# Performance work log

Measured on AMD Instinct MI355X. Metric: run time of the kernel, lower is better.

The kernel has to match this reference:

```python
import jax, jax.numpy as jnp
import numpy as np

NK, TH, SHARP, IMW, IMH = 9, 80.0, 2.0, 640.0, 480.0
NOOBJ, OBJ, COORD, CLS_SCALE, SIL = 1.0, 5.0, 1.0, 1.0, 0.6
NA, NC = 1, 13

def corner_conf(pr, gt):
    # pr, gt: [..., 9, 2] normalized corner coords
    scale = jnp.array([IMW, IMH], dtype=pr.dtype)
    d = (gt - pr) * scale
    dist = jnp.sqrt(jnp.sum(d * d, axis=-1))
    c = (jnp.exp(SHARP * (1.0 - dist / TH)) - 1.0) / (np.exp(SHARP) - 1.0)
    return jnp.where(dist < TH, c, 0.0).mean(axis=-1)

def build_targets(pc, target, nH, nW):
    # pc: [nB, nA*nH*nW, 9, 2] detached predicted corners (layout anchor-major, matching torch flatten)
    nB = target.shape[0]
    nL = 2 * NK + 3
    tgt = target.reshape(nB, 50, nL)
    # break on first slot with coord==0 -> valid prefix
    valid = jnp.cumprod((tgt[:, :, 1] != 0).astype(jnp.int32), axis=1).astype(bool)
    gt_c = tgt[:, :, 1:1 + 2 * NK].reshape(nB, 50, NK, 2)
    confs = corner_conf(pc[:, None], gt_c[:, :, None])  # [nB, 50, nAnch]
    cur = jnp.max(jnp.where(valid[:, :, None], confs, 0.0), axis=1)  # running max over targets
    conf_mask = jnp.where(cur > SIL, 0.0, NOOBJ).reshape(nB, NA, nH, nW)
    gi = (tgt[:, :, 1] * nW).astype(jnp.int32)  # int() truncation, coords in (0,1)
    gj = (tgt[:, :, 2] * nH).astype(jnp.int32)
    coord_mask = jnp.zeros((nB, NA, nH, nW), target.dtype)
    cls_mask = jnp.zeros((nB, NA, nH, nW), target.dtype)
    tcls = jnp.zeros((nB, NA, nH, nW), target.dtype)
    b = jnp.arange(nB)
    for t in range(50):  # fixed 50-slot buffer; sequential overwrite preserved
        git = jnp.where(valid[:, t], gi[:, t], nW)  # invalid -> OOB index, dropped
        gjt = gj[:, t]
        coord_mask = coord_mask.at[b, 0, gjt, git].set(1.0, mode='drop')
        conf_mask = conf_mask.at[b, 0, gjt, git].set(OBJ, mode='drop')
        cls_mask = cls_mask.at[b, 0, gjt, git].set(1.0, mode='drop')
        tcls = tcls.at[b, 0, gjt, git].set(tgt[:, t, 0], mode='drop')
    return coord_mask, conf_mask, cls_mask, tcls

def forward(output, distiled_target, target):
    nB, _, nH, nW = output.shape
    out = output.reshape(nB, NA, 19 + NC, nH, nW)
    coords = jnp.concatenate([jax.nn.sigmoid(out[:, :, :2]), out[:, :, 2:18]], axis=2)
    conf = jax.nn.sigmoid(out[:, :, 18])
    cls_logits = out[:, :, 19:]  # [nB, nA, nC, nH, nW]
    gx = jnp.arange(nW, dtype=output.dtype)
    gy = jnp.arange(nH, dtype=output.dtype)
    px = (coords[:, :, 0::2] + gx[None, None, None, None, :]) / nW  # [nB,NA,9,nH,nW]
    py = (coords[:, :, 1::2] + gy[None, None, None, :, None]) / nH
    pc = jnp.stack([px, py], axis=-1)  # [nB,NA,9,nH,nW,2]
    pc = jnp.transpose(pc, (0, 1, 3, 4, 2, 5)).reshape(nB, NA * nH * nW, NK, 2)
    pc = jax.lax.stop_gradient(pc)  # torch uses .data (detached) for build_targets
    coord_mask, conf_mask, cls_mask, tcls = build_targets(pc, target, nH, nW)
    # distilled (teacher) targets replace build_targets' tx*/ty*/tconf
    dt = distiled_target.reshape(nB, NA, 19 + NC, nH, nW)
    tcoords = jnp.concatenate([jax.nn.sigmoid(dt[:, :, :2]), dt[:, :, 2:18]], axis=2)
    tconf = jax.nn.sigmoid(dt[:, :, 18])
    cm = coord_mask[:, :, None]  # broadcast over 18 coord channels
    loss_coord = COORD * 0.5 * jnp.sum(((coords - tcoords) * cm) ** 2)
    loss_conf = 0.5 * jnp.sum(((conf - tconf) * jnp.sqrt(conf_mask)) ** 2)
    logp = jax.nn.log_softmax(cls_logits, axis=2)
    ce = -jnp.take_along_axis(logp, tcls.astype(jnp.int32)[:, :, None], axis=2)[:, :, 0]
    loss_cls = CLS_SCALE * jnp.sum(cls_mask * ce)  # CrossEntropyLoss(size_average=False) on masked cells
    return loss_coord + loss_conf + loss_cls

def setup_inputs():
    key = jax.random.key(0)
    k1, k2, k3, k4 = jax.random.split(key, 4)
    nB, nH, nW = 16, 76, 76
    output = jax.random.normal(k1, (nB, NA * (19 + NC), nH, nW), dtype=jnp.float32)
    distiled_target = jax.random.normal(k2, (nB, NA * (19 + NC), nH, nW), dtype=jnp.float32)
    nL = 2 * NK + 3
    target = jax.random.uniform(k3, (nB, 50 * nL), dtype=jnp.float32, minval=0.02, maxval=0.98)
    cls_col = jax.random.randint(k4, (nB, 50), 0, NC).astype(jnp.float32)
    target = target.at[:, 0::nL].set(cls_col)
    target = target.at[:, 20 * nL:].set(0.0)  # 20 valid objects per image
    return {"output": output, "distiled_target": distiled_target, "target": target}

def reference(output, distiled_target, target):
    return forward(output, distiled_target, target)
```

## Files before the change

kernel.cpp:

```cpp
#include <hip/hip_runtime.h>
#include <math.h>

#define NB    16
#define NH    76
#define NW    76
#define NCELL (NH * NW)
#define NCH   32
#define NKP   9
#define NCLS  13
#define NT    50
#define NLROW 21
#define BLOCK 256
#define CPB   ((NCELL + BLOCK - 1) / BLOCK)

#define INV_EM1 0.15651764274966565f

__device__ __forceinline__ float sigmoidf_(float x) {
    return 1.0f / (1.0f + __expf(-x));
}

__global__ __launch_bounds__(BLOCK) void loss_main(
    const float* __restrict__ out,
    const float* __restrict__ dt,
    const float* __restrict__ tgt,
    float* __restrict__ partial)
{
    __shared__ float sraw[NT * NLROW];
    __shared__ float sgtx[NT * NKP];
    __shared__ float sgty[NT * NKP];
    __shared__ int   sgi[NT], sgj[NT], scls[NT];
    __shared__ int   snv;
    __shared__ float swsum[BLOCK / 64];

    const int b   = blockIdx.y;
    const int tid = threadIdx.x;

    for (int i = tid; i < NT * NLROW; i += BLOCK)
        sraw[i] = tgt[b * NT * NLROW + i];
    __syncthreads();

    if (tid < NT) {
        sgi[tid] = (int)(sraw[tid * NLROW + 1] * (float)NW);
        sgj[tid] = (int)(sraw[tid * NLROW + 2] * (float)NH);
        int c = (int)sraw[tid * NLROW + 0];
        scls[tid] = min(max(c, 0), NCLS - 1);
    }
    if (tid < NT * NKP) {
        int t = tid / NKP, k = tid - t * NKP;
        sgtx[tid] = sraw[t * NLROW + 1 + 2 * k] * 640.0f;
        sgty[tid] = sraw[t * NLROW + 2 + 2 * k] * 480.0f;
    }
    if (tid == 0) {
        int nv = 0;
        while (nv < NT && sraw[nv * NLROW + 1] != 0.0f) nv++;
        snv = nv;
    }
    __syncthreads();

    const int cell = blockIdx.x * BLOCK + tid;
    float total = 0.0f;

    if (cell < NCELL) {
        const int j = cell / NW;
        const int i = cell - j * NW;
        const float fi = (float)i, fj = (float)j;

        const float* ob = out + (size_t)b * NCH * NCELL + cell;
        const float* db = dt  + (size_t)b * NCH * NCELL + cell;

        float px[NKP], py[NKP];
        #pragma unroll
        for (int k = 0; k < NKP; k++) {
            float cx = ob[(2 * k)     * NCELL];
            float cy = ob[(2 * k + 1) * NCELL];
            if (k == 0) { cx = sigmoidf_(cx); cy = sigmoidf_(cy); }
            px[k] = (cx + fi) * (640.0f / 76.0f);
            py[k] = (cy + fj) * (480.0f / 76.0f);
        }
        const float conf  = sigmoidf_(ob[18 * NCELL]);
        const float tconf = sigmoidf_(db[18 * NCELL]);

        const int nv = snv;
        float cur = 0.0f;
        int flag = 0, tcls = 0;
        for (int t = 0; t < nv; t++) {
            if (sgi[t] == i && sgj[t] == j) { flag = 1; tcls = scls[t]; }
            float s = 0.0f;
            #pragma unroll
            for (int k = 0; k < NKP; k++) {
                float dx = sgtx[t * NKP + k] - px[k];
                float dy = sgty[t * NKP + k] - py[k];
                float dist = sqrtf(dx * dx + dy * dy);
                float c = (__expf(2.0f - dist * 0.025f) - 1.0f) * INV_EM1;
                s += (dist < 80.0f) ? c : 0.0f;
            }
            cur = fmaxf(cur, s * (1.0f / 9.0f));
        }

        const float cmask = flag ? 5.0f : (cur > 0.6f ? 0.0f : 1.0f);
        const float dcf = conf - tconf;
        total = 0.5f * dcf * dcf * cmask;

        if (flag) {
            float cl = 0.0f;
            #pragma unroll
            for (int ch = 0; ch < 18; ch++) {
                float a  = ob[ch * NCELL];
                float bb = db[ch * NCELL];
                if (ch < 2) { a = sigmoidf_(a); bb = sigmoidf_(bb); }
                float d = a - bb;
                cl += d * d;
            }
            total += 0.5f * cl;

            float cv[NCLS];
            float mx = -1e30f;
            #pragma unroll
            for (int c2 = 0; c2 < NCLS; c2++) {
                cv[c2] = ob[(19 + c2) * NCELL];
                mx = fmaxf(mx, cv[c2]);
            }
            float se = 0.0f;
            #pragma unroll
            for (int c2 = 0; c2 < NCLS; c2++) se += __expf(cv[c2] - mx);
            float lse = mx + __logf(se);
            total += lse - cv[tcls];
        }
    }

    #pragma unroll
    for (int off = 32; off > 0; off >>= 1)
        total += __shfl_down(total, off, 64);
    if ((tid & 63) == 0) swsum[tid >> 6] = total;
    __syncthreads();
    if (tid == 0) {
        float s = 0.0f;
        #pragma unroll
        for (int w = 0; w < BLOCK / 64; w++) s += swsum[w];
        partial[b * CPB + blockIdx.x] = s;
    }
}

__global__ __launch_bounds__(512) void reduce_partial(
    const float* __restrict__ partial, float* __restrict__ outp, int n)
{
    __shared__ float sw[8];
    const int tid = threadIdx.x;
    float v = 0.0f;
    for (int i = tid; i < n; i += 512) v += partial[i];
    #pragma unroll
    for (int off = 32; off > 0; off >>= 1)
        v += __shfl_down(v, off, 64);
    if ((tid & 63) == 0) sw[tid >> 6] = v;
    __syncthreads();
    if (tid == 0) {
        float s = 0.0f;
        #pragma unroll
        for (int w = 0; w < 8; w++) s += sw[w];
        outp[0] = s;
    }
}

extern "C" void kernel_launch(void* const* d_in, const int* in_sizes, int n_in,
                              void* d_out, int out_size, void* d_ws, size_t ws_size,
                              hipStream_t stream) {
    const float* out_p = (const float*)d_in[0];
    const float* dt_p  = (const float*)d_in[1];
    const float* tgt_p = (const float*)d_in[2];
    float* partial = (float*)d_ws;

    dim3 grid(CPB, NB);
    loss_main<<<grid, BLOCK, 0, stream>>>(out_p, dt_p, tgt_p, partial);
    reduce_partial<<<1, 512, 0, stream>>>(partial, (float*)d_out, NB * CPB);
}
```

Before: 93.77 us.

## Read targets directly from global memory with single-wave blocks, dropping LDS staging

Shrinks the block to one 64-thread wavefront and removes the shared-memory staging of the target table and its barriers. Each thread now reads target rows straight from global memory (uniform addresses, cache-served) and computes grid indices and scaled corners inline. The valid-count scan becomes an early break. The block reduction becomes a single wave shuffle, and the final reducer drops to 256 threads. The trade is that per-thread work in the inner loop grows: scalar or cached loads and extra multiplies replace LDS reads, against more blocks with no barrier stalls.

```diff
diff --git a/kernel.cpp b/kernel.cpp
--- a/kernel.cpp
+++ b/kernel.cpp
@@ -10,7 +10,7 @@
 #define NCLS  13
 #define NT    50
 #define NLROW 21
-#define BLOCK 256
+#define BLOCK 64
 #define CPB   ((NCELL + BLOCK - 1) / BLOCK)
 
 #define INV_EM1 0.15651764274966565f
@@ -25,39 +25,12 @@
     const float* __restrict__ tgt,
     float* __restrict__ partial)
 {
-    __shared__ float sraw[NT * NLROW];
-    __shared__ float sgtx[NT * NKP];
-    __shared__ float sgty[NT * NKP];
-    __shared__ int   sgi[NT], sgj[NT], scls[NT];
-    __shared__ int   snv;
-    __shared__ float swsum[BLOCK / 64];
+    const int b    = blockIdx.y;
+    const int tid  = threadIdx.x;
+    const int cell = blockIdx.x * BLOCK + tid;
 
-    const int b   = blockIdx.y;
-    const int tid = threadIdx.x;
+    const float* __restrict__ trow = tgt + (size_t)b * NT * NLROW;
 
-    for (int i = tid; i < NT * NLROW; i += BLOCK)
-        sraw[i] = tgt[b * NT * NLROW + i];
-    __syncthreads();
-
-    if (tid < NT) {
-        sgi[tid] = (int)(sraw[tid * NLROW + 1] * (float)NW);
-        sgj[tid] = (int)(sraw[tid * NLROW + 2] * (float)NH);
-        int c = (int)sraw[tid * NLROW + 0];
-        scls[tid] = min(max(c, 0), NCLS - 1);
-    }
-    if (tid < NT * NKP) {
-        int t = tid / NKP, k = tid - t * NKP;
-        sgtx[tid] = sraw[t * NLROW + 1 + 2 * k] * 640.0f;
-        sgty[tid] = sraw[t * NLROW + 2 + 2 * k] * 480.0f;
-    }
-    if (tid == 0) {
-        int nv = 0;
-        while (nv < NT && sraw[nv * NLROW + 1] != 0.0f) nv++;
-        snv = nv;
-    }
-    __syncthreads();
-
-    const int cell = blockIdx.x * BLOCK + tid;
     float total = 0.0f;
 
     if (cell < NCELL) {
@@ -68,30 +41,40 @@
         const float* ob = out + (size_t)b * NCH * NCELL + cell;
         const float* db = dt  + (size_t)b * NCH * NCELL + cell;
 
-        float px[NKP], py[NKP];
+        float pxn[NKP], pyn[NKP];
         #pragma unroll
         for (int k = 0; k < NKP; k++) {
             float cx = ob[(2 * k)     * NCELL];
             float cy = ob[(2 * k + 1) * NCELL];
             if (k == 0) { cx = sigmoidf_(cx); cy = sigmoidf_(cy); }
-            px[k] = (cx + fi) * (640.0f / 76.0f);
-            py[k] = (cy + fj) * (480.0f / 76.0f);
+            pxn[k] = (cx + fi) * (1.0f / 76.0f);
+            pyn[k] = (cy + fj) * (1.0f / 76.0f);
         }
         const float conf  = sigmoidf_(ob[18 * NCELL]);
         const float tconf = sigmoidf_(db[18 * NCELL]);
 
-        const int nv = snv;
         float cur = 0.0f;
         int flag = 0, tcls = 0;
-        for (int t = 0; t < nv; t++) {
-            if (sgi[t] == i && sgj[t] == j) { flag = 1; tcls = scls[t]; }
+        for (int t = 0; t < NT; t++) {
+            const float x0 = trow[t * NLROW + 1];
+            if (x0 == 0.0f) break;
+            const float y0 = trow[t * NLROW + 2];
+            const int gi = (int)(x0 * (float)NW);
+            const int gj = (int)(y0 * (float)NH);
+            if (gi == i && gj == j) {
+                flag = 1;
+                int c = (int)trow[t * NLROW + 0];
+                tcls = min(max(c, 0), NCLS - 1);
+            }
             float s = 0.0f;
             #pragma unroll
             for (int k = 0; k < NKP; k++) {
-                float dx = sgtx[t * NKP + k] - px[k];
-                float dy = sgty[t * NKP + k] - py[k];
-                float dist = sqrtf(dx * dx + dy * dy);
-                float c = (__expf(2.0f - dist * 0.025f) - 1.0f) * INV_EM1;
+                const float gx = trow[t * NLROW + 1 + 2 * k];
+                const float gy = trow[t * NLROW + 2 + 2 * k];
+                const float dx = (gx - pxn[k]) * 640.0f;
+                const float dy = (gy - pyn[k]) * 480.0f;
+                const float dist = sqrtf(dx * dx + dy * dy);
+                const float c = (__expf(2.0f - dist * 0.025f) - 1.0f) * INV_EM1;
                 s += (dist < 80.0f) ? c : 0.0f;
             }
             cur = fmaxf(cur, s * (1.0f / 9.0f));
@@ -131,23 +114,17 @@
     #pragma unroll
     for (int off = 32; off > 0; off >>= 1)
         total += __shfl_down(total, off, 64);
-    if ((tid & 63) == 0) swsum[tid >> 6] = total;
-    __syncthreads();
-    if (tid == 0) {
-        float s = 0.0f;
-        #pragma unroll
-        for (int w = 0; w < BLOCK / 64; w++) s += swsum[w];
-        partial[b * CPB + blockIdx.x] = s;
-    }
+    if (tid == 0)
+        partial[b * CPB + blockIdx.x] = total;
 }
 
-__global__ __launch_bounds__(512) void reduce_partial(
+__global__ __launch_bounds__(256) void reduce_partial(
     const float* __restrict__ partial, float* __restrict__ outp, int n)
 {
-    __shared__ float sw[8];
+    __shared__ float sw[4];
     const int tid = threadIdx.x;
     float v = 0.0f;
-    for (int i = tid; i < n; i += 512) v += partial[i];
+    for (int i = tid; i < n; i += 256) v += partial[i];
     #pragma unroll
     for (int off = 32; off > 0; off >>= 1)
         v += __shfl_down(v, off, 64);
@@ -156,7 +133,7 @@
     if (tid == 0) {
         float s = 0.0f;
         #pragma unroll
-        for (int w = 0; w < 8; w++) s += sw[w];
+        for (int w = 0; w < 4; w++) s += sw[w];
         outp[0] = s;
     }
 }
@@ -171,5 +148,5 @@
 
     dim3 grid(CPB, NB);
     loss_main<<<grid, BLOCK, 0, stream>>>(out_p, dt_p, tgt_p, partial);
-    reduce_partial<<<1, 512, 0, stream>>>(partial, (float*)d_out, NB * CPB);
+    reduce_partial<<<1, 256, 0, stream>>>(partial, (float*)d_out, NB * CPB);
 }
```

Measured after the change: 94.31 us. No clear change (+0.6%).
